# Performance work log

Measured on AMD Instinct MI355X. Metric: run time of the kernel, lower is better.

The kernel has to match this reference:

```python
import jax, jax.numpy as jnp
import numpy as np

DIM = 384
NUM_HEADS = 12
WIN = (8, 8, 8)
Q_TOK = 1
K_TOK = 1
B = 64
N = WIN[0] * WIN[1] * WIN[2]  # 512


def _build_rel_index():
    t = max(Q_TOK, K_TOK)
    max_rel = [(w - 1) * t for w in WIN]
    nbins = [2 * m + 1 for m in max_rel]
    def coords(tok):
        axes = [np.arange(WIN[i]) * tok for i in range(3)]
        g = np.stack(np.meshgrid(*axes, indexing='ij'))  # [3, D, H, W]
        return g.reshape(3, -1)  # [3, N]
    cq = coords(Q_TOK)
    ck = coords(K_TOK)
    rel = (cq[:, :, None] - ck[:, None, :]).transpose(1, 2, 0)  # [N, N, 3]
    rel = rel + np.array(max_rel)
    idx = rel[..., 0] * (nbins[1] * nbins[2]) + rel[..., 1] * nbins[2] + rel[..., 2]
    return idx.astype(np.int32), nbins[0] * nbins[1] * nbins[2]


def setup_inputs() -> dict:
    key = jax.random.key(0)
    ks = jax.random.split(key, 7)
    rel_index_np, num_rel = _build_rel_index()
    s = 0.02
    return {
        'x1': jax.random.normal(ks[0], (B, N, DIM), jnp.float32),
        'x2': jax.random.normal(ks[1], (B, N, DIM), jnp.float32),
        'Wq': jax.random.normal(ks[2], (DIM, DIM), jnp.float32) * s,
        'Wkv': jax.random.normal(ks[3], (2 * DIM, DIM), jnp.float32) * s,
        'q_bias': jax.random.normal(ks[4], (DIM,), jnp.float32) * s,
        'v_bias': jax.random.normal(ks[5], (DIM,), jnp.float32) * s,
        'bias_table': jax.random.normal(ks[6], (num_rel, NUM_HEADS), jnp.float32) * s,
        'rel_index': jnp.asarray(rel_index_np),  # [N, N] int32
    }


def reference(x1, x2, Wq, Wkv, q_bias, v_bias, bias_table, rel_index):
    Bq, N1, C = x1.shape
    N2 = x2.shape[1]
    H = NUM_HEADS
    hd = C // H

    q = x1 @ Wq.T + q_bias                      # [B, N1, C]
    kv_bias = jnp.concatenate([jnp.zeros_like(v_bias), v_bias])
    kv = x2 @ Wkv.T + kv_bias                   # [B, N2, 2C]

    q = q.reshape(Bq, N1, H, hd).transpose(0, 2, 1, 3)   # [B, H, N1, hd]
    kv = kv.reshape(Bq, N2, 2, H, hd).transpose(2, 0, 3, 1, 4)
    k, v = kv[0], kv[1]                          # [B, H, N2, hd]

    # relative position bias: gather [N1, N2, H] -> [H, N1, N2]
    bias = bias_table[rel_index]                 # [N1, N2, H]
    bias = bias.transpose(2, 0, 1)               # [H, N1, N2]

    scale = 1.0 / jnp.sqrt(jnp.asarray(hd, q.dtype))
    scores = jnp.einsum('bhqd,bhkd->bhqk', q, k) * scale + bias[None]
    attn = jax.nn.softmax(scores, axis=-1)
    out = jnp.einsum('bhqk,bhkd->bhqd', attn, v)  # [B, H, N1, hd]
    return out.transpose(0, 2, 1, 3).reshape(Bq, N1, C)
```

## Files before the change

kernel.cpp:

```cpp
#include <hip/hip_runtime.h>

typedef unsigned short u16;
typedef unsigned int u32;
typedef __bf16 bf16x8 __attribute__((ext_vector_type(8)));
typedef float f32x4 __attribute__((ext_vector_type(4)));
typedef u16 u16x8 __attribute__((ext_vector_type(8)));
typedef u32 u32x4 __attribute__((ext_vector_type(4)));

#define NB 64
#define NN 512
#define NH 12
#define HD 32
#define DIM 384

static constexpr size_t QWS = (size_t)NB * NH * NN * HD;
#define LOG2E 1.4426950408889634f
#define QSCALE 0.25503486f

__device__ __forceinline__ u16 f2bf(float f) {
  __bf16 b = (__bf16)f;
  union { __bf16 b; u16 u; } v; v.b = b;
  return v.u;
}
__device__ __forceinline__ float lo16f(u32 w) {
  union { u32 u; float f; } v; v.u = w << 16;
  return v.f;
}
__device__ __forceinline__ float hi16f(u32 w) {
  union { u32 u; float f; } v; v.u = w & 0xffff0000u;
  return v.f;
}
__device__ __forceinline__ void gload16(const void* g, void* l) {
  __builtin_amdgcn_global_load_lds((const __attribute__((address_space(1))) u32*)g,
                                   (__attribute__((address_space(3))) u32*)l, 16, 0, 0);
}

__global__ __launch_bounds__(256) void prep_k(const float* __restrict__ table,
                                              const int* __restrict__ rel,
                                              const float* __restrict__ Wq,
                                              const float* __restrict__ Wkv,
                                              u32* __restrict__ beR,
                                              u16* __restrict__ Wf) {
  int bid = blockIdx.x;
  if (bid < 6144) {
    int t = bid * 256 + threadIdx.x;
    int word = t & 3;
    int lane = (t >> 2) & 63;
    int mf   = (t >> 8) & 3;
    int wv   = (t >> 10) & 7;
    int kt   = (t >> 13) & 15;
    int h    = t >> 17;
    int lr = lane & 15, lg = lane >> 4;
    int q = wv * 64 + mf * 16 + lr;
    int k = kt * 32 + (word >> 1) * 16 + lg * 4 + (word & 1) * 2;
    int i0 = rel[q * NN + k];
    int i1 = rel[q * NN + k + 1];
    u16 b0 = f2bf(table[i0 * NH + h] * LOG2E);
    u16 b1 = f2bf(table[i1 * NH + h] * LOG2E);
    beR[t] = (u32)b0 | ((u32)b1 << 16);
  } else {
    int t2 = (bid - 6144) * 256 + threadIdx.x;
    int lane = t2 & 63;
    int kk = (t2 >> 6) % 12;
    int cb = t2 / (12 * 64);
    int j = cb * 16 + (lane & 15);
    int k = kk * 32 + (lane >> 4) * 8;
    const float* wrow = (j < 384) ? (Wq + (size_t)j * DIM) : (Wkv + (size_t)(j - 384) * DIM);
    float4 a = *(const float4*)(wrow + k);
    float4 b = *(const float4*)(wrow + k + 4);
    u16x8 o = {f2bf(a.x), f2bf(a.y), f2bf(a.z), f2bf(a.w),
               f2bf(b.x), f2bf(b.y), f2bf(b.z), f2bf(b.w)};
    *(u16x8*)(Wf + (size_t)t2 * 8) = o;
  }
}

__global__ __launch_bounds__(512, 6) void qkv_proj_k(const float* __restrict__ x1,
                                                     const float* __restrict__ x2,
                                                     const float* __restrict__ qb,
                                                     const float* __restrict__ vb,
                                                     const u16* __restrict__ Wf,
                                                     u16* __restrict__ q_ws,
                                                     u16* __restrict__ k_ws,
                                                     u16* __restrict__ v_ws) {
  __shared__ __attribute__((aligned(16))) u16 Wbuf[2][12288];

  const int g = blockIdx.x;
  const int vv = (g & 7) * 96 + (g >> 3);
  const int type = vv >> 8;
  const int m0 = (vv & 255) * 128;
  const int tid = threadIdx.x, lane = tid & 63, w = tid >> 6;
  const int lg = lane >> 4, lr = lane & 15;
  const float* X = (type == 0) ? x1 : x2;
  const int cb0 = type * 24;
  const char* wsrc = (const char*)(Wf + (size_t)cb0 * 12 * 64 * 8);
  const int bb = m0 >> 9;

  bf16x8 af[12];
  const float* xrow = X + (size_t)(m0 + w * 16 + lr) * DIM + lg * 8;
#pragma unroll
  for (int kk = 0; kk < 12; ++kk) {
    float4 a = *(const float4*)(xrow + kk * 32);
    float4 b = *(const float4*)(xrow + kk * 32 + 4);
    af[kk] = (bf16x8){(__bf16)a.x, (__bf16)a.y, (__bf16)a.z, (__bf16)a.w,
                      (__bf16)b.x, (__bf16)b.y, (__bf16)b.z, (__bf16)b.w};
  }

#pragma unroll
  for (int i = 0; i < 3; ++i) {
    int inst = w + i * 8;
    gload16(wsrc + inst * 1024 + lane * 16, (char*)&Wbuf[0][0] + inst * 1024 + lane * 16);
  }
  __syncthreads();

  u16* dst = (type == 0) ? q_ws : (type == 1 ? k_ws : v_ws);
  const float scale = (type == 0) ? QSCALE : 1.0f;
  const int rowb = (m0 & 511) + w * 16 + lg * 4;

  for (int c = 0; c < 12; ++c) {
    if (c + 1 < 12) {
      const char* s = wsrc + (size_t)(c + 1) * 24576;
      char* d = (char*)&Wbuf[(c + 1) & 1][0];
#pragma unroll
      for (int i = 0; i < 3; ++i) {
        int inst = w + i * 8;
        gload16(s + inst * 1024 + lane * 16, d + inst * 1024 + lane * 16);
      }
    }
    const u16* wb = &Wbuf[c & 1][0];
    f32x4 acc0 = {0.f, 0.f, 0.f, 0.f};
    f32x4 acc1 = {0.f, 0.f, 0.f, 0.f};
#pragma unroll
    for (int kk = 0; kk < 12; ++kk) {
      bf16x8 wf0 = *(const bf16x8*)(wb + (kk * 64 + lane) * 8);
      bf16x8 wf1 = *(const bf16x8*)(wb + ((12 + kk) * 64 + lane) * 8);
      acc0 = __builtin_amdgcn_mfma_f32_16x16x32_bf16(af[kk], wf0, acc0, 0, 0, 0);
      acc1 = __builtin_amdgcn_mfma_f32_16x16x32_bf16(af[kk], wf1, acc1, 0, 0, 0);
    }
#pragma unroll
    for (int lc = 0; lc < 2; ++lc) {
      f32x4 acc = lc ? acc1 : acc0;
      int j = (cb0 + c * 2 + lc) * 16 + lr;
      int jj = (type == 0) ? j : (type == 1 ? j - 384 : j - 768);
      float bv = (type == 0) ? qb[jj] : (type == 2 ? vb[jj] : 0.0f);
      int hh = jj >> 5, dd = jj & 31;
      size_t basead = ((size_t)(bb * NH + hh) * NN) * HD + dd;
#pragma unroll
      for (int r = 0; r < 4; ++r)
        dst[basead + (size_t)(rowb + r) * HD] = f2bf((acc[r] + bv) * scale);
    }
    __syncthreads();
  }
}

__global__ __launch_bounds__(512, 4) void attn_k(const u16* __restrict__ qw,
                                                 const u16* __restrict__ kw,
                                                 const u16* __restrict__ vw,
                                                 const u32* __restrict__ beR,
                                                 float* __restrict__ out) {
  const int g = blockIdx.x;
  const int vv = (g & 7) * 96 + (g >> 3);
  const int h = vv >> 6, b = vv & 63;
  const size_t base = ((size_t)b * NH + h) * NN * HD;
  const u16* Q = qw + base;
  const u16* K = kw + base;
  const u16* V = vw + base;

  __shared__ u16 Ks[NN][40];
  __shared__ u16 Vtp[HD][520];

  const int tid = threadIdx.x;
  const int lane = tid & 63, w = tid >> 6;
  const int lg = lane >> 4, lr = lane & 15;
  const int q0 = w * 64;

  bf16x8 qf[4];
#pragma unroll
  for (int mf = 0; mf < 4; ++mf)
    qf[mf] = *(const bf16x8*)&Q[(q0 + mf * 16 + lr) * HD + lg * 8];

  for (int c = tid; c < 2048; c += 512) {
    int row = c >> 2, part = (c & 3) * 8;
    *(u16x8*)&Ks[row][part] = *(const u16x8*)&K[row * HD + part];
    u16x8 vld = *(const u16x8*)&V[row * HD + part];
    int kk = row & 31;
    int col = (row & ~31) + ((kk >> 2) & 3) * 8 + (kk >> 4) * 4 + (kk & 3);
#pragma unroll
    for (int j = 0; j < 8; ++j) Vtp[part + j][col] = vld[j];
  }
  __syncthreads();

  const u32* bstream = beR + ((((size_t)h * 16) * 8 + w) * 4) * 256 + lane * 4;

  f32x4 accOT[4][2] = {};
  float lsum[4] = {0.f, 0.f, 0.f, 0.f};

  for (int kt = 0; kt < 16; ++kt) {
    const int k0 = kt * 32;
    const u32* bkt = bstream + (size_t)kt * 8192;
    bf16x8 kf0 = *(const bf16x8*)&Ks[k0 + lr][lg * 8];
    bf16x8 kf1 = *(const bf16x8*)&Ks[k0 + 16 + lr][lg * 8];
    bf16x8 vp0 = *(const bf16x8*)&Vtp[lr][k0 + lg * 8];
    bf16x8 vp1 = *(const bf16x8*)&Vtp[16 + lr][k0 + lg * 8];
#pragma unroll
    for (int mf = 0; mf < 4; ++mf) {
      u32x4 bbv = *(const u32x4*)(bkt + mf * 256);
      f32x4 c0 = {lo16f(bbv.x), hi16f(bbv.x), lo16f(bbv.y), hi16f(bbv.y)};
      f32x4 c1 = {lo16f(bbv.z), hi16f(bbv.z), lo16f(bbv.w), hi16f(bbv.w)};
      f32x4 s0 = __builtin_amdgcn_mfma_f32_16x16x32_bf16(kf0, qf[mf], c0, 0, 0, 0);
      f32x4 s1 = __builtin_amdgcn_mfma_f32_16x16x32_bf16(kf1, qf[mf], c1, 0, 0, 0);
      float p0[4], p1[4];
#pragma unroll
      for (int r = 0; r < 4; ++r) {
        p0[r] = __builtin_amdgcn_exp2f(s0[r]);
        p1[r] = __builtin_amdgcn_exp2f(s1[r]);
      }
      lsum[mf] += ((p0[0] + p0[1]) + (p0[2] + p0[3])) +
                  ((p1[0] + p1[1]) + (p1[2] + p1[3]));
      bf16x8 pv = {(__bf16)p0[0], (__bf16)p0[1], (__bf16)p0[2], (__bf16)p0[3],
                   (__bf16)p1[0], (__bf16)p1[1], (__bf16)p1[2], (__bf16)p1[3]};
      accOT[mf][0] = __builtin_amdgcn_mfma_f32_16x16x32_bf16(vp0, pv, accOT[mf][0], 0, 0, 0);
      accOT[mf][1] = __builtin_amdgcn_mfma_f32_16x16x32_bf16(vp1, pv, accOT[mf][1], 0, 0, 0);
    }
  }

  float linv[4];
#pragma unroll
  for (int mf = 0; mf < 4; ++mf) {
    float s = lsum[mf];
    s += __shfl_xor(s, 16, 64);
    s += __shfl_xor(s, 32, 64);
    linv[mf] = 1.0f / s;
  }

  float* outp = out + ((size_t)b * NN) * DIM + h * HD;
#pragma unroll
  for (int mf = 0; mf < 4; ++mf) {
    int q = q0 + mf * 16 + lr;
#pragma unroll
    for (int nf = 0; nf < 2; ++nf) {
      float4 o = {accOT[mf][nf][0] * linv[mf], accOT[mf][nf][1] * linv[mf],
                  accOT[mf][nf][2] * linv[mf], accOT[mf][nf][3] * linv[mf]};
      *(float4*)&outp[(size_t)q * DIM + nf * 16 + lg * 4] = o;
    }
  }
}

extern "C" void kernel_launch(void* const* d_in, const int* in_sizes, int n_in,
                              void* d_out, int out_size, void* d_ws, size_t ws_size,
                              hipStream_t stream) {
  const float* x1    = (const float*)d_in[0];
  const float* x2    = (const float*)d_in[1];
  const float* Wq    = (const float*)d_in[2];
  const float* Wkv   = (const float*)d_in[3];
  const float* qb    = (const float*)d_in[4];
  const float* vb    = (const float*)d_in[5];
  const float* table = (const float*)d_in[6];
  const int*   rel   = (const int*)d_in[7];
  float* out = (float*)d_out;

  u16* ws   = (u16*)d_ws;
  u16* q_ws = ws;
  u16* k_ws = ws + QWS;
  u16* v_ws = ws + 2 * QWS;
  u32* beR  = (u32*)(ws + 3 * QWS);
  u16* Wf   = ws + 3 * QWS + 2 * 1572864;

  prep_k<<<6360, 256, 0, stream>>>(table, rel, Wq, Wkv, beR, Wf);
  qkv_proj_k<<<768, 512, 0, stream>>>(x1, x2, qb, vb, Wf, q_ws, k_ws, v_ws);
  attn_k<<<NB * NH, 512, 0, stream>>>(q_ws, k_ws, v_ws, beR, out);
}
```

Baseline: 113.4 us.

## Switch QKV projection to 32x32x16 MFMA with 4-wave blocks

Rewrites the QKV projection GEMM to use 32x32x16 bf16 MFMA tiles instead of two 16x16x32 tiles, with 256-thread blocks where each wave owns 32 rows. The weight pre-swizzle in the prep kernel is changed to match the new fragment layout. Each chunk now maps to exactly one head, which simplifies the bias and store addressing and gives better operand reuse per MFMA. In exchange each thread holds 24 A fragments plus a 16-wide accumulator, raising register pressure, and halving the threads per block changes occupancy and the per-thread LDS load count.

```diff
diff --git a/kernel.cpp b/kernel.cpp
--- a/kernel.cpp
+++ b/kernel.cpp
@@ -4,6 +4,7 @@
 typedef unsigned int u32;
 typedef __bf16 bf16x8 __attribute__((ext_vector_type(8)));
 typedef float f32x4 __attribute__((ext_vector_type(4)));
+typedef float f32x16 __attribute__((ext_vector_type(16)));
 typedef u16 u16x8 __attribute__((ext_vector_type(8)));
 typedef u32 u32x4 __attribute__((ext_vector_type(4)));
 
@@ -61,10 +62,10 @@
   } else {
     int t2 = (bid - 6144) * 256 + threadIdx.x;
     int lane = t2 & 63;
-    int kk = (t2 >> 6) % 12;
-    int cb = t2 / (12 * 64);
-    int j = cb * 16 + (lane & 15);
-    int k = kk * 32 + (lane >> 4) * 8;
+    int kk = (t2 >> 6) % 24;
+    int cb = t2 / (24 * 64);
+    int j = cb * 32 + (lane & 31);
+    int k = kk * 16 + (lane >> 5) * 8;
     const float* wrow = (j < 384) ? (Wq + (size_t)j * DIM) : (Wkv + (size_t)(j - 384) * DIM);
     float4 a = *(const float4*)(wrow + k);
     float4 b = *(const float4*)(wrow + k + 4);
@@ -74,7 +75,7 @@
   }
 }
 
-__global__ __launch_bounds__(512, 6) void qkv_proj_k(const float* __restrict__ x1,
+__global__ __launch_bounds__(256, 2) void qkv_proj_k(const float* __restrict__ x1,
                                                      const float* __restrict__ x2,
                                                      const float* __restrict__ qb,
                                                      const float* __restrict__ vb,
@@ -89,64 +90,54 @@
   const int type = vv >> 8;
   const int m0 = (vv & 255) * 128;
   const int tid = threadIdx.x, lane = tid & 63, w = tid >> 6;
-  const int lg = lane >> 4, lr = lane & 15;
+  const int lo = lane & 31, hi = lane >> 5;
   const float* X = (type == 0) ? x1 : x2;
-  const int cb0 = type * 24;
-  const char* wsrc = (const char*)(Wf + (size_t)cb0 * 12 * 64 * 8);
-  const int bb = m0 >> 9;
-
-  bf16x8 af[12];
-  const float* xrow = X + (size_t)(m0 + w * 16 + lr) * DIM + lg * 8;
-#pragma unroll
-  for (int kk = 0; kk < 12; ++kk) {
-    float4 a = *(const float4*)(xrow + kk * 32);
-    float4 b = *(const float4*)(xrow + kk * 32 + 4);
+  const int bb = m0 >> 9, m0r = m0 & 511;
+  const char* wsrc = (const char*)(Wf + (size_t)type * 12 * 12288);
+
+  bf16x8 af[24];
+  const float* xrow = X + (size_t)(m0 + w * 32 + lo) * DIM + hi * 8;
+#pragma unroll
+  for (int kk = 0; kk < 24; ++kk) {
+    float4 a = *(const float4*)(xrow + kk * 16);
+    float4 b = *(const float4*)(xrow + kk * 16 + 4);
     af[kk] = (bf16x8){(__bf16)a.x, (__bf16)a.y, (__bf16)a.z, (__bf16)a.w,
                       (__bf16)b.x, (__bf16)b.y, (__bf16)b.z, (__bf16)b.w};
   }
 
 #pragma unroll
-  for (int i = 0; i < 3; ++i) {
-    int inst = w + i * 8;
+  for (int i = 0; i < 6; ++i) {
+    int inst = w * 6 + i;
     gload16(wsrc + inst * 1024 + lane * 16, (char*)&Wbuf[0][0] + inst * 1024 + lane * 16);
   }
   __syncthreads();
 
   u16* dst = (type == 0) ? q_ws : (type == 1 ? k_ws : v_ws);
   const float scale = (type == 0) ? QSCALE : 1.0f;
-  const int rowb = (m0 & 511) + w * 16 + lg * 4;
 
   for (int c = 0; c < 12; ++c) {
     if (c + 1 < 12) {
       const char* s = wsrc + (size_t)(c + 1) * 24576;
       char* d = (char*)&Wbuf[(c + 1) & 1][0];
 #pragma unroll
-      for (int i = 0; i < 3; ++i) {
-        int inst = w + i * 8;
+      for (int i = 0; i < 6; ++i) {
+        int inst = w * 6 + i;
         gload16(s + inst * 1024 + lane * 16, d + inst * 1024 + lane * 16);
       }
     }
     const u16* wb = &Wbuf[c & 1][0];
-    f32x4 acc0 = {0.f, 0.f, 0.f, 0.f};
-    f32x4 acc1 = {0.f, 0.f, 0.f, 0.f};
-#pragma unroll
-    for (int kk = 0; kk < 12; ++kk) {
-      bf16x8 wf0 = *(const bf16x8*)(wb + (kk * 64 + lane) * 8);
-      bf16x8 wf1 = *(const bf16x8*)(wb + ((12 + kk) * 64 + lane) * 8);
-      acc0 = __builtin_amdgcn_mfma_f32_16x16x32_bf16(af[kk], wf0, acc0, 0, 0, 0);
-      acc1 = __builtin_amdgcn_mfma_f32_16x16x32_bf16(af[kk], wf1, acc1, 0, 0, 0);
-    }
-#pragma unroll
-    for (int lc = 0; lc < 2; ++lc) {
-      f32x4 acc = lc ? acc1 : acc0;
-      int j = (cb0 + c * 2 + lc) * 16 + lr;
-      int jj = (type == 0) ? j : (type == 1 ? j - 384 : j - 768);
-      float bv = (type == 0) ? qb[jj] : (type == 2 ? vb[jj] : 0.0f);
-      int hh = jj >> 5, dd = jj & 31;
-      size_t basead = ((size_t)(bb * NH + hh) * NN) * HD + dd;
-#pragma unroll
-      for (int r = 0; r < 4; ++r)
-        dst[basead + (size_t)(rowb + r) * HD] = f2bf((acc[r] + bv) * scale);
+    f32x16 acc = {};
+#pragma unroll
+    for (int kk = 0; kk < 24; ++kk) {
+      bf16x8 wf = *(const bf16x8*)(wb + kk * 512 + lane * 8);
+      acc = __builtin_amdgcn_mfma_f32_32x32x16_bf16(af[kk], wf, acc, 0, 0, 0);
+    }
+    float bv = (type == 0) ? qb[c * 32 + lo] : (type == 2 ? vb[c * 32 + lo] : 0.0f);
+    u16* dbase = dst + (((size_t)(bb * NH + c) * NN) + m0r + w * 32) * HD + lo;
+#pragma unroll
+    for (int reg = 0; reg < 16; ++reg) {
+      int row = (reg & 3) + 8 * (reg >> 2) + 4 * hi;
+      dbase[(size_t)row * HD] = f2bf((acc[reg] + bv) * scale);
     }
     __syncthreads();
   }
@@ -266,6 +257,6 @@
   u16* Wf   = ws + 3 * QWS + 2 * 1572864;
 
   prep_k<<<6360, 256, 0, stream>>>(table, rel, Wq, Wkv, beR, Wf);
-  qkv_proj_k<<<768, 512, 0, stream>>>(x1, x2, qb, vb, Wf, q_ws, k_ws, v_ws);
+  qkv_proj_k<<<768, 256, 0, stream>>>(x1, x2, qb, vb, Wf, q_ws, k_ws, v_ws);
   attn_k<<<NB * NH, 512, 0, stream>>>(q_ws, k_ws, v_ws, beR, out);
 }
```

Result: no change. 113.6 us (+0.2%).

## Give each QKV projection wave two row tiles and vectorize transposed output stores

Applied to the files above, without the earlier changes.

The projection kernel now runs 256-thread blocks in which each wave computes 32 rows instead of 16. Each LDS weight fragment is therefore reused across two MFMA row tiles, which halves LDS weight reads per output. The MFMA operands are swapped so the accumulator holds 4 consecutive head-dim values per lane. That allows 8-byte vector stores and float4 bias loads in place of scattered 2-byte stores. The trade-off is higher register pressure (24 A fragments) and fewer threads per block to hide latency.

```diff
diff --git a/kernel.cpp b/kernel.cpp
--- a/kernel.cpp
+++ b/kernel.cpp
@@ -4,6 +4,7 @@
 typedef unsigned int u32;
 typedef __bf16 bf16x8 __attribute__((ext_vector_type(8)));
 typedef float f32x4 __attribute__((ext_vector_type(4)));
+typedef u16 u16x4 __attribute__((ext_vector_type(4)));
 typedef u16 u16x8 __attribute__((ext_vector_type(8)));
 typedef u32 u32x4 __attribute__((ext_vector_type(4)));
 
@@ -74,7 +75,7 @@
   }
 }
 
-__global__ __launch_bounds__(512, 6) void qkv_proj_k(const float* __restrict__ x1,
+__global__ __launch_bounds__(256, 3) void qkv_proj_k(const float* __restrict__ x1,
                                                      const float* __restrict__ x2,
                                                      const float* __restrict__ qb,
                                                      const float* __restrict__ vb,
@@ -91,62 +92,74 @@
   const int tid = threadIdx.x, lane = tid & 63, w = tid >> 6;
   const int lg = lane >> 4, lr = lane & 15;
   const float* X = (type == 0) ? x1 : x2;
-  const int cb0 = type * 24;
-  const char* wsrc = (const char*)(Wf + (size_t)cb0 * 12 * 64 * 8);
-  const int bb = m0 >> 9;
-
-  bf16x8 af[12];
-  const float* xrow = X + (size_t)(m0 + w * 16 + lr) * DIM + lg * 8;
-#pragma unroll
-  for (int kk = 0; kk < 12; ++kk) {
-    float4 a = *(const float4*)(xrow + kk * 32);
-    float4 b = *(const float4*)(xrow + kk * 32 + 4);
-    af[kk] = (bf16x8){(__bf16)a.x, (__bf16)a.y, (__bf16)a.z, (__bf16)a.w,
-                      (__bf16)b.x, (__bf16)b.y, (__bf16)b.z, (__bf16)b.w};
-  }
-
-#pragma unroll
-  for (int i = 0; i < 3; ++i) {
-    int inst = w + i * 8;
-    gload16(wsrc + inst * 1024 + lane * 16, (char*)&Wbuf[0][0] + inst * 1024 + lane * 16);
+  const int bb = m0 >> 9, m0r = m0 & 511;
+  const char* wsrc = (const char*)(Wf + (size_t)type * 24 * 6144);
+
+  bf16x8 aflo[12], afhi[12];
+  {
+    const float* xlo = X + (size_t)(m0 + w * 32 + lr) * DIM + lg * 8;
+    const float* xhi = xlo + (size_t)16 * DIM;
+#pragma unroll
+    for (int kk = 0; kk < 12; ++kk) {
+      float4 a = *(const float4*)(xlo + kk * 32);
+      float4 b = *(const float4*)(xlo + kk * 32 + 4);
+      aflo[kk] = (bf16x8){(__bf16)a.x, (__bf16)a.y, (__bf16)a.z, (__bf16)a.w,
+                          (__bf16)b.x, (__bf16)b.y, (__bf16)b.z, (__bf16)b.w};
+      float4 c = *(const float4*)(xhi + kk * 32);
+      float4 d = *(const float4*)(xhi + kk * 32 + 4);
+      afhi[kk] = (bf16x8){(__bf16)c.x, (__bf16)c.y, (__bf16)c.z, (__bf16)c.w,
+                          (__bf16)d.x, (__bf16)d.y, (__bf16)d.z, (__bf16)d.w};
+    }
+  }
+
+#pragma unroll
+  for (int i = 0; i < 6; ++i) {
+    int off = (i * 256 + tid) * 16;
+    gload16(wsrc + off, (char*)&Wbuf[0][0] + off);
   }
   __syncthreads();
 
   u16* dst = (type == 0) ? q_ws : (type == 1 ? k_ws : v_ws);
+  const float* bias = (type == 0) ? qb : (type == 2 ? vb : nullptr);
   const float scale = (type == 0) ? QSCALE : 1.0f;
-  const int rowb = (m0 & 511) + w * 16 + lg * 4;
 
   for (int c = 0; c < 12; ++c) {
     if (c + 1 < 12) {
       const char* s = wsrc + (size_t)(c + 1) * 24576;
       char* d = (char*)&Wbuf[(c + 1) & 1][0];
 #pragma unroll
-      for (int i = 0; i < 3; ++i) {
-        int inst = w + i * 8;
-        gload16(s + inst * 1024 + lane * 16, d + inst * 1024 + lane * 16);
+      for (int i = 0; i < 6; ++i) {
+        int off = (i * 256 + tid) * 16;
+        gload16(s + off, d + off);
       }
     }
     const u16* wb = &Wbuf[c & 1][0];
-    f32x4 acc0 = {0.f, 0.f, 0.f, 0.f};
-    f32x4 acc1 = {0.f, 0.f, 0.f, 0.f};
+    f32x4 acc[2][2] = {};
 #pragma unroll
     for (int kk = 0; kk < 12; ++kk) {
       bf16x8 wf0 = *(const bf16x8*)(wb + (kk * 64 + lane) * 8);
       bf16x8 wf1 = *(const bf16x8*)(wb + ((12 + kk) * 64 + lane) * 8);
-      acc0 = __builtin_amdgcn_mfma_f32_16x16x32_bf16(af[kk], wf0, acc0, 0, 0, 0);
-      acc1 = __builtin_amdgcn_mfma_f32_16x16x32_bf16(af[kk], wf1, acc1, 0, 0, 0);
+      acc[0][0] = __builtin_amdgcn_mfma_f32_16x16x32_bf16(wf0, aflo[kk], acc[0][0], 0, 0, 0);
+      acc[0][1] = __builtin_amdgcn_mfma_f32_16x16x32_bf16(wf0, afhi[kk], acc[0][1], 0, 0, 0);
+      acc[1][0] = __builtin_amdgcn_mfma_f32_16x16x32_bf16(wf1, aflo[kk], acc[1][0], 0, 0, 0);
+      acc[1][1] = __builtin_amdgcn_mfma_f32_16x16x32_bf16(wf1, afhi[kk], acc[1][1], 0, 0, 0);
     }
 #pragma unroll
     for (int lc = 0; lc < 2; ++lc) {
-      f32x4 acc = lc ? acc1 : acc0;
-      int j = (cb0 + c * 2 + lc) * 16 + lr;
-      int jj = (type == 0) ? j : (type == 1 ? j - 384 : j - 768);
-      float bv = (type == 0) ? qb[jj] : (type == 2 ? vb[jj] : 0.0f);
-      int hh = jj >> 5, dd = jj & 31;
-      size_t basead = ((size_t)(bb * NH + hh) * NN) * HD + dd;
-#pragma unroll
-      for (int r = 0; r < 4; ++r)
-        dst[basead + (size_t)(rowb + r) * HD] = f2bf((acc[r] + bv) * scale);
+      int cb = c * 2 + lc;
+      int head = cb >> 1;
+      int d0 = (cb & 1) * 16 + lg * 4;
+      float4 bv = {0.f, 0.f, 0.f, 0.f};
+      if (type != 1) bv = *(const float4*)(bias + head * 32 + d0);
+#pragma unroll
+      for (int rg = 0; rg < 2; ++rg) {
+        int n = m0r + w * 32 + rg * 16 + lr;
+        u16x4 o = {f2bf((acc[lc][rg][0] + bv.x) * scale),
+                   f2bf((acc[lc][rg][1] + bv.y) * scale),
+                   f2bf((acc[lc][rg][2] + bv.z) * scale),
+                   f2bf((acc[lc][rg][3] + bv.w) * scale)};
+        *(u16x4*)(dst + ((size_t)(bb * NH + head) * NN + n) * HD + d0) = o;
+      }
     }
     __syncthreads();
   }
@@ -266,6 +279,6 @@
   u16* Wf   = ws + 3 * QWS + 2 * 1572864;
 
   prep_k<<<6360, 256, 0, stream>>>(table, rel, Wq, Wkv, beR, Wf);
-  qkv_proj_k<<<768, 512, 0, stream>>>(x1, x2, qb, vb, Wf, q_ws, k_ws, v_ws);
+  qkv_proj_k<<<768, 256, 0, stream>>>(x1, x2, qb, vb, Wf, q_ws, k_ws, v_ws);
   attn_k<<<NB * NH, 512, 0, stream>>>(q_ws, k_ws, v_ws, beR, out);
 }
```

After: 111.7 us. No clear change (-1.5%).

## Retile QKV projection to stage a 128-column weight slab per block

Applied to the files above, without the earlier changes.

The QKV projection is restructured so each block owns one batch and a 128-output-column group. The block loads the full 96KB bf16 weight slice for that group into LDS once, instead of streaming 12 double-buffered chunks with a barrier per chunk. The MFMA operands are swapped so each lane's accumulator holds 4 consecutive head-dim values, which allows vectorized 8-byte stores and a float4 bias load in place of scalar strided stores. The trade-off is that x rows are now re-read from global memory by 3 column-group blocks, and the large LDS footprint limits occupancy to about one block per CU.

```diff
diff --git a/kernel.cpp b/kernel.cpp
--- a/kernel.cpp
+++ b/kernel.cpp
@@ -4,6 +4,7 @@
 typedef unsigned int u32;
 typedef __bf16 bf16x8 __attribute__((ext_vector_type(8)));
 typedef float f32x4 __attribute__((ext_vector_type(4)));
+typedef u16 u16x4 __attribute__((ext_vector_type(4)));
 typedef u16 u16x8 __attribute__((ext_vector_type(8)));
 typedef u32 u32x4 __attribute__((ext_vector_type(4)));
 
@@ -61,9 +62,11 @@
   } else {
     int t2 = (bid - 6144) * 256 + threadIdx.x;
     int lane = t2 & 63;
-    int kk = (t2 >> 6) % 12;
-    int cb = t2 / (12 * 64);
-    int j = cb * 16 + (lane & 15);
+    int cb   = (t2 >> 6) & 7;
+    int kk   = (t2 >> 9) % 12;
+    int tcbg = t2 / 6144;
+    int type = tcbg / 3, cbg = tcbg % 3;
+    int j = type * 384 + (cbg * 8 + cb) * 16 + (lane & 15);
     int k = kk * 32 + (lane >> 4) * 8;
     const float* wrow = (j < 384) ? (Wq + (size_t)j * DIM) : (Wkv + (size_t)(j - 384) * DIM);
     float4 a = *(const float4*)(wrow + k);
@@ -74,7 +77,7 @@
   }
 }
 
-__global__ __launch_bounds__(512, 6) void qkv_proj_k(const float* __restrict__ x1,
+__global__ __launch_bounds__(512, 1) void qkv_proj_k(const float* __restrict__ x1,
                                                      const float* __restrict__ x2,
                                                      const float* __restrict__ qb,
                                                      const float* __restrict__ vb,
@@ -82,73 +85,62 @@
                                                      u16* __restrict__ q_ws,
                                                      u16* __restrict__ k_ws,
                                                      u16* __restrict__ v_ws) {
-  __shared__ __attribute__((aligned(16))) u16 Wbuf[2][12288];
+  __shared__ __attribute__((aligned(16))) u16 Ws[49152];
 
   const int g = blockIdx.x;
-  const int vv = (g & 7) * 96 + (g >> 3);
-  const int type = vv >> 8;
-  const int m0 = (vv & 255) * 128;
+  const int vv = (g & 7) * 72 + (g >> 3);
+  const int tcbg = vv / 64;
+  const int b = vv & 63;
+  const int type = tcbg / 3, cbg = tcbg % 3;
   const int tid = threadIdx.x, lane = tid & 63, w = tid >> 6;
   const int lg = lane >> 4, lr = lane & 15;
   const float* X = (type == 0) ? x1 : x2;
-  const int cb0 = type * 24;
-  const char* wsrc = (const char*)(Wf + (size_t)cb0 * 12 * 64 * 8);
-  const int bb = m0 >> 9;
-
-  bf16x8 af[12];
-  const float* xrow = X + (size_t)(m0 + w * 16 + lr) * DIM + lg * 8;
-#pragma unroll
-  for (int kk = 0; kk < 12; ++kk) {
-    float4 a = *(const float4*)(xrow + kk * 32);
-    float4 b = *(const float4*)(xrow + kk * 32 + 4);
-    af[kk] = (bf16x8){(__bf16)a.x, (__bf16)a.y, (__bf16)a.z, (__bf16)a.w,
-                      (__bf16)b.x, (__bf16)b.y, (__bf16)b.z, (__bf16)b.w};
-  }
-
-#pragma unroll
-  for (int i = 0; i < 3; ++i) {
-    int inst = w + i * 8;
-    gload16(wsrc + inst * 1024 + lane * 16, (char*)&Wbuf[0][0] + inst * 1024 + lane * 16);
+
+  const char* wsrc = (const char*)(Wf + (size_t)tcbg * 49152);
+#pragma unroll
+  for (int i = 0; i < 12; ++i) {
+    int off = (i * 512 + tid) * 16;
+    gload16(wsrc + off, (char*)Ws + off);
   }
   __syncthreads();
 
   u16* dst = (type == 0) ? q_ws : (type == 1 ? k_ws : v_ws);
+  const float* bias = (type == 0) ? qb : (type == 2 ? vb : nullptr);
   const float scale = (type == 0) ? QSCALE : 1.0f;
-  const int rowb = (m0 & 511) + w * 16 + lg * 4;
-
-  for (int c = 0; c < 12; ++c) {
-    if (c + 1 < 12) {
-      const char* s = wsrc + (size_t)(c + 1) * 24576;
-      char* d = (char*)&Wbuf[(c + 1) & 1][0];
-#pragma unroll
-      for (int i = 0; i < 3; ++i) {
-        int inst = w + i * 8;
-        gload16(s + inst * 1024 + lane * 16, d + inst * 1024 + lane * 16);
+
+  for (int s = 0; s < 4; ++s) {
+    const int n = w * 64 + s * 16 + lr;
+    bf16x8 af[12];
+    const float* xrow = X + ((size_t)b * NN + n) * DIM + lg * 8;
+#pragma unroll
+    for (int kk = 0; kk < 12; ++kk) {
+      float4 a = *(const float4*)(xrow + kk * 32);
+      float4 c = *(const float4*)(xrow + kk * 32 + 4);
+      af[kk] = (bf16x8){(__bf16)a.x, (__bf16)a.y, (__bf16)a.z, (__bf16)a.w,
+                        (__bf16)c.x, (__bf16)c.y, (__bf16)c.z, (__bf16)c.w};
+    }
+    f32x4 acc[8] = {};
+#pragma unroll
+    for (int kk = 0; kk < 12; ++kk) {
+#pragma unroll
+      for (int cb = 0; cb < 8; ++cb) {
+        bf16x8 wf = *(const bf16x8*)(Ws + ((kk * 8 + cb) * 64 + lane) * 8);
+        acc[cb] = __builtin_amdgcn_mfma_f32_16x16x32_bf16(wf, af[kk], acc[cb], 0, 0, 0);
       }
     }
-    const u16* wb = &Wbuf[c & 1][0];
-    f32x4 acc0 = {0.f, 0.f, 0.f, 0.f};
-    f32x4 acc1 = {0.f, 0.f, 0.f, 0.f};
-#pragma unroll
-    for (int kk = 0; kk < 12; ++kk) {
-      bf16x8 wf0 = *(const bf16x8*)(wb + (kk * 64 + lane) * 8);
-      bf16x8 wf1 = *(const bf16x8*)(wb + ((12 + kk) * 64 + lane) * 8);
-      acc0 = __builtin_amdgcn_mfma_f32_16x16x32_bf16(af[kk], wf0, acc0, 0, 0, 0);
-      acc1 = __builtin_amdgcn_mfma_f32_16x16x32_bf16(af[kk], wf1, acc1, 0, 0, 0);
-    }
-#pragma unroll
-    for (int lc = 0; lc < 2; ++lc) {
-      f32x4 acc = lc ? acc1 : acc0;
-      int j = (cb0 + c * 2 + lc) * 16 + lr;
-      int jj = (type == 0) ? j : (type == 1 ? j - 384 : j - 768);
-      float bv = (type == 0) ? qb[jj] : (type == 2 ? vb[jj] : 0.0f);
-      int hh = jj >> 5, dd = jj & 31;
-      size_t basead = ((size_t)(bb * NH + hh) * NN) * HD + dd;
-#pragma unroll
-      for (int r = 0; r < 4; ++r)
-        dst[basead + (size_t)(rowb + r) * HD] = f2bf((acc[r] + bv) * scale);
-    }
-    __syncthreads();
+#pragma unroll
+    for (int cb = 0; cb < 8; ++cb) {
+      int cbt = cbg * 8 + cb;
+      int head = cbt >> 1;
+      int d0 = (cbt & 1) * 16 + lg * 4;
+      float4 bv = {0.f, 0.f, 0.f, 0.f};
+      if (type != 1) bv = *(const float4*)(bias + head * 32 + d0);
+      u16x4 o = {f2bf((acc[cb][0] + bv.x) * scale),
+                 f2bf((acc[cb][1] + bv.y) * scale),
+                 f2bf((acc[cb][2] + bv.z) * scale),
+                 f2bf((acc[cb][3] + bv.w) * scale)};
+      *(u16x4*)(dst + ((size_t)(b * NH + head) * NN + n) * HD + d0) = o;
+    }
   }
 }
 
@@ -266,6 +258,6 @@
   u16* Wf   = ws + 3 * QWS + 2 * 1572864;
 
   prep_k<<<6360, 256, 0, stream>>>(table, rel, Wq, Wkv, beR, Wf);
-  qkv_proj_k<<<768, 512, 0, stream>>>(x1, x2, qb, vb, Wf, q_ws, k_ws, v_ws);
+  qkv_proj_k<<<576, 512, 0, stream>>>(x1, x2, qb, vb, Wf, q_ws, k_ws, v_ws);
   attn_k<<<NB * NH, 512, 0, stream>>>(q_ws, k_ws, v_ws, beR, out);
 }
```

Result: slower. 451.8 us (+298.4%).
